# Kernel tuning notes

Measured on AMD Instinct MI355X. Metric: run time of the kernel, lower is better.

## Reference

```python
import jax, jax.numpy as jnp
import numpy as np


def setup_inputs() -> dict:
    key = jax.random.key(0)
    k1, k2, k3, k4 = jax.random.split(key, 4)
    B, S, D_IN, D_OUT = 4, 4096, 768, 128
    x = jax.random.normal(k1, (B, S, D_IN), dtype=jnp.float32)
    # torch Linear(d_in, d_out) weight is [d_out, d_in]; we store transposed [d_in, d_out]
    scale = 1.0 / np.sqrt(D_IN)
    Wq = jax.random.normal(k2, (D_IN, D_OUT), dtype=jnp.float32) * scale
    Wk = jax.random.normal(k3, (D_IN, D_OUT), dtype=jnp.float32) * scale
    Wv = jax.random.normal(k4, (D_IN, D_OUT), dtype=jnp.float32) * scale
    return {"x": x, "Wq": Wq, "Wk": Wk, "Wv": Wv}


def reference(x, Wq, Wk, Wv):
    # x: [B, S, d_in]; Wq/Wk/Wv: [d_in, d_out]
    B, S, _ = x.shape
    q = jnp.einsum('bsd,de->bse', x, Wq)
    k = jnp.einsum('bsd,de->bse', x, Wk)
    v = jnp.einsum('bsd,de->bse', x, Wv)
    d_out = k.shape[-1]
    scores = jnp.einsum('bqe,bke->bqk', q, k)  # [B, S, S]
    causal = jnp.tril(jnp.ones((S, S), dtype=bool))  # True where attention allowed
    scores = jnp.where(causal[None], scores, -jnp.inf)
    attn = jax.nn.softmax(scores / jnp.sqrt(jnp.float32(d_out)), axis=-1)
    # dropout prob is 0.0 -> identity
    return jnp.einsum('bqk,bke->bqe', attn, v)
```

## Files before the change

### kernel.cpp

```cpp
#include <hip/hip_runtime.h>
#include <stdint.h>

typedef unsigned short u16;
typedef uint32_t u32;
typedef __bf16 bf16;
typedef bf16 bf16x8 __attribute__((ext_vector_type(8)));
typedef bf16 bf16x4 __attribute__((ext_vector_type(4)));
typedef short s16x4 __attribute__((ext_vector_type(4)));
typedef float f32x4 __attribute__((ext_vector_type(4)));
typedef uint32_t u32x4 __attribute__((ext_vector_type(4)));

#define S_LEN 4096
#define D_IN 768
#define D_OUT 128
#define NB 4
#define M_TOTAL (NB * S_LEN)

static __device__ __forceinline__ u16 f2bf(float f) {
    union { float f; uint32_t u; } c; c.f = f;
    return (u16)((c.u + 0x7FFFu + ((c.u >> 16) & 1u)) >> 16);
}
static __device__ __forceinline__ float bf2f_lo(uint32_t w) { return __uint_as_float(w << 16); }
static __device__ __forceinline__ float bf2f_hi(uint32_t w) { return __uint_as_float(w & 0xFFFF0000u); }

static __device__ __forceinline__ bf16x8 ld8(const u16* p) {
    union { u32x4 v; bf16x8 b; } c;
    c.v = *reinterpret_cast<const u32x4*>(p);
    return c.b;
}

static __device__ __forceinline__ f32x4 mfma16(bf16x8 a, bf16x8 b, f32x4 c) {
    return __builtin_amdgcn_mfma_f32_16x16x32_bf16(a, b, c, 0, 0, 0);
}

static __device__ __forceinline__ f32x4 mfma16k16(uint2 a, uint2 b, f32x4 c) {
#if defined(__HIP_DEVICE_COMPILE__)
#if __has_builtin(__builtin_amdgcn_mfma_f32_16x16x16_bf16)
    union { uint2 u; bf16x4 v; } ca, cb; ca.u = a; cb.u = b;
    return __builtin_amdgcn_mfma_f32_16x16x16_bf16(ca.v, cb.v, c, 0, 0, 0);
#else
    union { uint2 u; s16x4 v; } ca, cb; ca.u = a; cb.u = b;
    return __builtin_amdgcn_mfma_f32_16x16x16bf16_1k(ca.v, cb.v, c, 0, 0, 0);
#endif
#else
    (void)a; (void)b;
    return c;
#endif
}

static __device__ __forceinline__ void gload16(const void* g, void* l) {
    __builtin_amdgcn_global_load_lds((const __attribute__((address_space(1))) uint32_t*)g,
                                     (__attribute__((address_space(3))) uint32_t*)l, 16, 0, 0);
}

static __device__ __forceinline__ float bpermf(int addr, float v) {
    return __int_as_float(__builtin_amdgcn_ds_bpermute(addr, __float_as_int(v)));
}
static __device__ __forceinline__ u32 pk2(float a, float b) {
    return __builtin_amdgcn_perm(__float_as_uint(b), __float_as_uint(a), 0x07060302u);
}

__global__ __launch_bounds__(256) void wt_kernel(const float* __restrict__ Wq, const float* __restrict__ Wk,
                                                 const float* __restrict__ Wv, u16* __restrict__ Wt) {
    __shared__ u16 tl[128][40];
    const int w = blockIdx.x / 24;
    const int kc = (blockIdx.x % 24) * 32;
    const float* W = (w == 0) ? Wq : (w == 1) ? Wk : Wv;
#pragma unroll
    for (int p = 0; p < 4; ++p) {
        int kr = p * 8 + (threadIdx.x >> 5);
        int nc = (threadIdx.x & 31) * 4;
        float4 v = *reinterpret_cast<const float4*>(W + (size_t)(kc + kr) * D_OUT + nc);
        tl[nc + 0][kr] = f2bf(v.x); tl[nc + 1][kr] = f2bf(v.y);
        tl[nc + 2][kr] = f2bf(v.z); tl[nc + 3][kr] = f2bf(v.w);
    }
    __syncthreads();
    const int n = threadIdx.x >> 1, kh = (threadIdx.x & 1) * 16;
    u32x4* dst = reinterpret_cast<u32x4*>(Wt + (size_t)w * D_OUT * D_IN + (size_t)n * D_IN + kc + kh);
    const u32x4* src = reinterpret_cast<const u32x4*>(&tl[n][kh]);
    dst[0] = src[0];
    dst[1] = src[1];
}

__global__ __launch_bounds__(256) void qkv_kernel(const float* __restrict__ x, const u16* __restrict__ Wt,
                                                  u16* __restrict__ Qb, u16* __restrict__ Kb,
                                                  u16* __restrict__ Vt) {
    __shared__ __align__(16) u16 wslab[2][192 * 32];
    __shared__ __align__(16) float xslab[2][64 * 32];
    const int wave = threadIdx.x >> 6, lane = threadIdx.x & 63;
    const int r = lane & 15, g = lane >> 4;
    const int m0 = blockIdx.x * 64;
    const int h = blockIdx.y;

    f32x4 acc[3][4];
#pragma unroll
    for (int y = 0; y < 3; ++y)
#pragma unroll
        for (int f = 0; f < 4; ++f) acc[y][f] = f32x4{0.f, 0.f, 0.f, 0.f};

    auto stageW = [&](int bb, int kk) {
#pragma unroll
        for (int i = 0; i < 3; ++i) {
            int c = i * 4 + wave;
            int rr = c * 16 + (lane >> 2);
            int gr = (rr >> 6) * 128 + h * 64 + (rr & 63);
            const u16* src = Wt + (size_t)gr * D_IN + kk * 32 + (((lane & 3) ^ (rr & 3)) * 8);
            gload16(src, &wslab[bb][c * 512]);
        }
    };
    auto stageX = [&](int bb, int kk) {
#pragma unroll
        for (int i = 0; i < 2; ++i) {
            int c = i * 4 + wave;
            int row = c * 8 + (lane >> 3);
            const float* src = x + (size_t)(m0 + row) * D_IN + kk * 32 + (((lane & 7) ^ (row & 7)) * 4);
            gload16(src, &xslab[bb][c * 256]);
        }
    };

    stageW(0, 0);
    stageX(0, 0);
    int buf = 0;
    const int arow = wave * 16 + r;
    for (int kk = 0; kk < 24; ++kk) {
        int kn = (kk + 1 < 24) ? kk + 1 : 0;
        stageX(buf ^ 1, kn);
        stageW(buf ^ 1, kn);
        asm volatile("s_waitcnt vmcnt(5)" ::: "memory");
        __builtin_amdgcn_sched_barrier(0);
        __builtin_amdgcn_s_barrier();
        f32x4 xa0 = *reinterpret_cast<const f32x4*>(&xslab[buf][arow * 32 + (((2 * g) ^ (arow & 7)) * 4)]);
        f32x4 xa1 = *reinterpret_cast<const f32x4*>(&xslab[buf][arow * 32 + (((2 * g + 1) ^ (arow & 7)) * 4)]);
        union { u16 u[8]; bf16x8 bv; } af;
#pragma unroll
        for (int t = 0; t < 4; ++t) { af.u[t] = f2bf(xa0[t]); af.u[4 + t] = f2bf(xa1[t]); }
#pragma unroll
        for (int y = 0; y < 3; ++y)
#pragma unroll
            for (int f = 0; f < 4; ++f) {
                int rr = y * 64 + f * 16 + r;
                bf16x8 wf = ld8(&wslab[buf][rr * 32 + ((g ^ (r & 3)) * 8)]);
                acc[y][f] = mfma16(af.bv, wf, acc[y][f]);
            }
        __builtin_amdgcn_s_barrier();
        buf ^= 1;
    }
    asm volatile("s_waitcnt vmcnt(0)" ::: "memory");

    const float QSC = 0.1275174366f;
#pragma unroll
    for (int f = 0; f < 4; ++f)
#pragma unroll
        for (int i = 0; i < 4; ++i) {
            int mrow = m0 + wave * 16 + 4 * g + i;
            int col = h * 64 + f * 16 + r;
            Qb[(size_t)mrow * D_OUT + col] = f2bf(acc[0][f][i] * QSC);
            Kb[(size_t)mrow * D_OUT + col] = f2bf(acc[1][f][i]);
            Vt[((size_t)((mrow >> 12) * D_OUT + col)) * S_LEN + (mrow & 4095)] = f2bf(acc[2][f][i]);
        }
}

__global__ __launch_bounds__(512, 2) void attn_kernel(const u16* __restrict__ Qb, const u16* __restrict__ Kb,
                                                      const u16* __restrict__ Vt, u16* __restrict__ Po,
                                                      float* __restrict__ Pml, float* __restrict__ out,
                                                      int nsplit) {
    __shared__ __align__(16) u16 kbuf[2][64 * 128];
    __shared__ __align__(16) u16 vbuf[2][128 * 64];

    const int wave = threadIdx.x >> 6, lane = threadIdx.x & 63;
    const int r = lane & 15, g = lane >> 4;
    const int n = (int)blockIdx.x;
    const int b = (n & 7) >> 1;
    const int rem = ((n >> 3) << 1) | (n & 1);
    const int s = rem >> 4;
    const int xh = rem & 15;
    const int t = (2 * s < nsplit) ? (15 - xh) : xh;
    const int nj = 4 * t + 4;
    if (s >= nj) return;
    const int qw0 = t * 256 + wave * 32;

    const u16* Kp = Kb + (size_t)b * S_LEN * D_OUT;
    const u16* Vp = Vt + (size_t)b * D_OUT * S_LEN;

    bf16x8 qf[2][4];
#pragma unroll
    for (int rb = 0; rb < 2; ++rb)
#pragma unroll
        for (int kk = 0; kk < 4; ++kk)
            qf[rb][kk] = ld8(Qb + ((size_t)(b * S_LEN + qw0 + rb * 16 + r)) * D_OUT + kk * 32 + 8 * g);

    f32x4 o[2][8];
    float l_[2];
#pragma unroll
    for (int rb = 0; rb < 2; ++rb) {
#pragma unroll
        for (int f = 0; f < 8; ++f) o[rb][f] = f32x4{0.f, 0.f, 0.f, 0.f};
        l_[rb] = 0.f;
    }

    const int lx16 = (lane ^ 16) * 4, lx32 = (lane ^ 32) * 4;

    auto stageK = [&](int bb, int k0) {
#pragma unroll
        for (int i = 0; i < 2; ++i) {
            int c = i * 8 + wave;
            int row = c * 4 + (lane >> 4);
            const u16* src = Kp + (size_t)(k0 + row) * D_OUT + (((lane & 15) ^ (row & 7)) * 8);
            gload16(src, &kbuf[bb][c * 512]);
        }
    };
    auto stageV = [&](int bb, int k0) {
#pragma unroll
        for (int i = 0; i < 2; ++i) {
            int c = i * 8 + wave;
            int row = c * 8 + (lane >> 3);
            const u16* src = Vp + (size_t)row * S_LEN + k0 + (((lane & 7) ^ (row & 7)) * 8);
            gload16(src, &vbuf[bb][c * 512]);
        }
    };

    stageK(0, s * 64);
    stageV(0, s * 64);
    int buf = 0;
    for (int j = s; j < nj; j += nsplit) {
        const int k0 = j * 64;
        asm volatile("s_waitcnt vmcnt(0)" ::: "memory");
        __builtin_amdgcn_sched_barrier(0);
        __builtin_amdgcn_s_barrier();
        const int j2 = j + nsplit;
        if (j2 < nj) {
            stageK(buf ^ 1, j2 * 64);
            stageV(buf ^ 1, j2 * 64);
        }

        f32x4 sv[2][4];
#pragma unroll
        for (int rb = 0; rb < 2; ++rb)
#pragma unroll
            for (int f = 0; f < 4; ++f) sv[rb][f] = f32x4{0.f, 0.f, 0.f, 0.f};
        __builtin_amdgcn_s_setprio(1);
#pragma unroll
        for (int kk = 0; kk < 4; ++kk)
#pragma unroll
            for (int f = 0; f < 4; ++f) {
                bf16x8 kf = ld8(&kbuf[buf][(f * 16 + r) * 128 + (((kk * 4 + g) ^ (r & 7)) * 8)]);
                sv[0][f] = mfma16(kf, qf[0][kk], sv[0][f]);
                sv[1][f] = mfma16(kf, qf[1][kk], sv[1][f]);
            }
        __builtin_amdgcn_s_setprio(0);

        uint2 pb[2][4];
#pragma unroll
        for (int rb = 0; rb < 2; ++rb) {
            const int qrb = qw0 + rb * 16;
            const int q = qrb + r;
            if (k0 + 63 > qrb) {
#pragma unroll
                for (int f = 0; f < 4; ++f)
#pragma unroll
                    for (int i = 0; i < 4; ++i)
                        if (k0 + 16 * f + 4 * g + i > q) sv[rb][f][i] = -1e30f;
            }
            float r0 = 0.f;
#pragma unroll
            for (int f = 0; f < 4; ++f)
#pragma unroll
                for (int i = 0; i < 4; ++i) {
                    float p = __builtin_amdgcn_exp2f(sv[rb][f][i]);
                    sv[rb][f][i] = p;
                    r0 += p;
                }
            l_[rb] += r0;
#pragma unroll
            for (int kb = 0; kb < 4; ++kb) {
                pb[rb][kb].x = pk2(sv[rb][kb][0], sv[rb][kb][1]);
                pb[rb][kb].y = pk2(sv[rb][kb][2], sv[rb][kb][3]);
            }
        }

        __builtin_amdgcn_s_setprio(1);
#pragma unroll
        for (int kb = 0; kb < 4; ++kb) {
            const int vs = ((2 * kb + (g >> 1)) ^ (r & 7)) * 8 + 4 * (g & 1);
#pragma unroll
            for (int f = 0; f < 8; ++f) {
                uint2 vf = *reinterpret_cast<const uint2*>(&vbuf[buf][(f * 16 + r) * 64 + vs]);
                o[0][f] = mfma16k16(vf, pb[0][kb], o[0][f]);
                o[1][f] = mfma16k16(vf, pb[1][kb], o[1][f]);
            }
        }
        __builtin_amdgcn_s_setprio(0);
        buf ^= 1;
    }
    asm volatile("s_waitcnt vmcnt(0)" ::: "memory");

    l_[0] += bpermf(lx16, l_[0]);
    l_[1] += bpermf(lx16, l_[1]);
    l_[0] += bpermf(lx32, l_[0]);
    l_[1] += bpermf(lx32, l_[1]);

    if (nsplit == 1) {
#pragma unroll
        for (int rb = 0; rb < 2; ++rb) {
            float inv = 1.0f / l_[rb];
            float* orow = out + ((size_t)(b * S_LEN + qw0 + rb * 16 + r)) * D_OUT;
#pragma unroll
            for (int f = 0; f < 8; ++f) {
                float4 v;
                v.x = o[rb][f][0] * inv; v.y = o[rb][f][1] * inv;
                v.z = o[rb][f][2] * inv; v.w = o[rb][f][3] * inv;
                *reinterpret_cast<float4*>(orow + 16 * f + 4 * g) = v;
            }
        }
    } else {
        const int pt = (b * 16 + t) * nsplit + s;
        u16* po = Po + (size_t)pt * (256 * 128);
        float* pml = Pml + (size_t)pt * 512;
#pragma unroll
        for (int rb = 0; rb < 2; ++rb) {
            u16* chunk0 = po + (size_t)((wave * 2 + rb) * 8) * 256 + lane * 4;
#pragma unroll
            for (int f = 0; f < 8; ++f) {
                u32 w0 = (u32)f2bf(o[rb][f][0]) | ((u32)f2bf(o[rb][f][1]) << 16);
                u32 w1 = (u32)f2bf(o[rb][f][2]) | ((u32)f2bf(o[rb][f][3]) << 16);
                uint2 ww; ww.x = w0; ww.y = w1;
                *reinterpret_cast<uint2*>(chunk0 + f * 256) = ww;
            }
            if (g == 0) {
                const int row = wave * 32 + rb * 16 + r;
                pml[row * 2 + 0] = 0.f;
                pml[row * 2 + 1] = l_[rb];
            }
        }
    }
}

__global__ __launch_bounds__(256) void merge_kernel(const u16* __restrict__ Po, const float* __restrict__ Pml,
                                                    float* __restrict__ out, int nsplit) {
    const int gr = blockIdx.x * 16 + (threadIdx.x >> 4);
    const int c0 = (threadIdx.x & 15) * 8;
    const int b = gr >> 12, rr = gr & 4095;
    const int t = rr >> 8, row = rr & 255;
    const int ns = min(nsplit, 4 * t + 4);
    const size_t pbase = (size_t)(b * 16 + t) * nsplit;

    const int wv = row >> 5, rbm = (row >> 4) & 1, r_ = row & 15;
    const int fm = c0 >> 4, g0 = (c0 >> 2) & 3;
    const size_t coff = (size_t)((wv * 2 + rbm) * 8 + fm) * 256;

    float L = 0.f;
#pragma unroll
    for (int s = 0; s < 8; ++s)
        if (s < ns) L += Pml[(pbase + s) * 512 + row * 2 + 1];
    const float inv = 1.0f / L;

    float acc[8];
#pragma unroll
    for (int k = 0; k < 8; ++k) acc[k] = 0.f;
#pragma unroll
    for (int s = 0; s < 8; ++s) {
        if (s < ns) {
            const u16* chunk = Po + (pbase + s) * (256 * 128) + coff;
            uint2 pv0 = *reinterpret_cast<const uint2*>(chunk + (g0 * 16 + r_) * 4);
            uint2 pv1 = *reinterpret_cast<const uint2*>(chunk + ((g0 + 1) * 16 + r_) * 4);
            acc[0] += bf2f_lo(pv0.x); acc[1] += bf2f_hi(pv0.x);
            acc[2] += bf2f_lo(pv0.y); acc[3] += bf2f_hi(pv0.y);
            acc[4] += bf2f_lo(pv1.x); acc[5] += bf2f_hi(pv1.x);
            acc[6] += bf2f_lo(pv1.y); acc[7] += bf2f_hi(pv1.y);
        }
    }
    float* op = out + (size_t)gr * D_OUT + c0;
    float4 v0, v1;
    v0.x = acc[0] * inv; v0.y = acc[1] * inv; v0.z = acc[2] * inv; v0.w = acc[3] * inv;
    v1.x = acc[4] * inv; v1.y = acc[5] * inv; v1.z = acc[6] * inv; v1.w = acc[7] * inv;
    *reinterpret_cast<float4*>(op) = v0;
    *reinterpret_cast<float4*>(op + 4) = v1;
}

extern "C" void kernel_launch(void* const* d_in, const int* in_sizes, int n_in,
                              void* d_out, int out_size, void* d_ws, size_t ws_size,
                              hipStream_t stream) {
    const float* x  = (const float*)d_in[0];
    const float* Wq = (const float*)d_in[1];
    const float* Wk = (const float*)d_in[2];
    const float* Wv = (const float*)d_in[3];
    float* out = (float*)d_out;

    u16* Qb = (u16*)d_ws;
    u16* Kb = Qb + (size_t)M_TOTAL * D_OUT;
    u16* Vt = Kb + (size_t)M_TOTAL * D_OUT;
    u16* Wt = Vt + (size_t)M_TOTAL * D_OUT;

    const unsigned long long base = (3ULL * M_TOTAL * D_OUT + 3ULL * D_OUT * D_IN) * 2ULL;
    const unsigned long long per = 4325376ULL;
    int nsplit = 8;
    if (ws_size < base + 8ULL * per) nsplit = 4;
    if (ws_size < base + 4ULL * per) nsplit = 2;
    if (ws_size < base + 2ULL * per) nsplit = 1;

    u16* Po = Wt + (size_t)3 * D_OUT * D_IN;
    float* Pml = (float*)(Po + (size_t)nsplit * 2097152ULL);

    wt_kernel<<<72, 256, 0, stream>>>(Wq, Wk, Wv, Wt);
    qkv_kernel<<<dim3(256, 2), 256, 0, stream>>>(x, Wt, Qb, Kb, Vt);
    attn_kernel<<<16 * nsplit * NB, 512, 0, stream>>>(Qb, Kb, Vt, Po, Pml, out, nsplit);
    if (nsplit > 1)
        merge_kernel<<<M_TOTAL / 16, 256, 0, stream>>>(Po, Pml, out, nsplit);
}
```

Measured before the change: 96.19 us.

## Balance causal attention splits per query tile and halve QKV block rows

Attention work is now split per query tile with a variable number of KV splits that grows with tile index, set by lookup tables, for 115 blocks per batch. Before, every tile used a fixed nsplit and blocks that had no work exited early. This is meant to even out per-block work under the causal mask and fill the GPU better. Separately, the QKV projection kernel now uses 32-row blocks, with wave pairs splitting the output columns, which doubles the grid to improve occupancy. In exchange the merge kernel reads up to 13 partials for the deepest tiles, and the split path needs more workspace; with less workspace it falls back to an unsplit mode.

```diff
diff --git a/kernel.cpp b/kernel.cpp
--- a/kernel.cpp
+++ b/kernel.cpp
@@ -15,6 +15,16 @@
 #define D_OUT 128
 #define NB 4
 #define M_TOTAL (NB * S_LEN)
+#define NPROP 115
+
+__device__ const unsigned char SPLITS_T[16] = {1,2,3,4,4,5,6,7,8,8,9,10,11,12,12,13};
+__device__ const unsigned char OFF_T[16]    = {0,1,3,6,10,14,19,25,32,40,48,57,67,78,90,102};
+__device__ const unsigned char TILE_OF[NPROP] = {
+    0, 1,1, 2,2,2, 3,3,3,3, 4,4,4,4, 5,5,5,5,5, 6,6,6,6,6,6, 7,7,7,7,7,7,7,
+    8,8,8,8,8,8,8,8, 9,9,9,9,9,9,9,9, 10,10,10,10,10,10,10,10,10,
+    11,11,11,11,11,11,11,11,11,11, 12,12,12,12,12,12,12,12,12,12,12,
+    13,13,13,13,13,13,13,13,13,13,13,13, 14,14,14,14,14,14,14,14,14,14,14,14,
+    15,15,15,15,15,15,15,15,15,15,15,15,15};
 
 static __device__ __forceinline__ u16 f2bf(float f) {
     union { float f; uint32_t u; } c; c.f = f;
@@ -86,22 +96,22 @@
                                                   u16* __restrict__ Qb, u16* __restrict__ Kb,
                                                   u16* __restrict__ Vt) {
     __shared__ __align__(16) u16 wslab[2][192 * 32];
-    __shared__ __align__(16) float xslab[2][64 * 32];
+    __shared__ __align__(16) float xslab[2][32 * 32];
     const int wave = threadIdx.x >> 6, lane = threadIdx.x & 63;
     const int r = lane & 15, g = lane >> 4;
-    const int m0 = blockIdx.x * 64;
+    const int m0 = blockIdx.x * 32;
     const int h = blockIdx.y;
 
-    f32x4 acc[3][4];
+    f32x4 acc[3][2];
 #pragma unroll
     for (int y = 0; y < 3; ++y)
 #pragma unroll
-        for (int f = 0; f < 4; ++f) acc[y][f] = f32x4{0.f, 0.f, 0.f, 0.f};
+        for (int f = 0; f < 2; ++f) acc[y][f] = f32x4{0.f, 0.f, 0.f, 0.f};
 
     auto stageW = [&](int bb, int kk) {
 #pragma unroll
         for (int i = 0; i < 3; ++i) {
-            int c = i * 4 + wave;
+            int c = wave * 3 + i;
             int rr = c * 16 + (lane >> 2);
             int gr = (rr >> 6) * 128 + h * 64 + (rr & 63);
             const u16* src = Wt + (size_t)gr * D_IN + kk * 32 + (((lane & 3) ^ (rr & 3)) * 8);
@@ -109,24 +119,22 @@
         }
     };
     auto stageX = [&](int bb, int kk) {
-#pragma unroll
-        for (int i = 0; i < 2; ++i) {
-            int c = i * 4 + wave;
-            int row = c * 8 + (lane >> 3);
-            const float* src = x + (size_t)(m0 + row) * D_IN + kk * 32 + (((lane & 7) ^ (row & 7)) * 4);
-            gload16(src, &xslab[bb][c * 256]);
-        }
+        int c = wave;
+        int row = c * 8 + (lane >> 3);
+        const float* src = x + (size_t)(m0 + row) * D_IN + kk * 32 + (((lane & 7) ^ (row & 7)) * 4);
+        gload16(src, &xslab[bb][c * 256]);
     };
 
     stageW(0, 0);
     stageX(0, 0);
     int buf = 0;
-    const int arow = wave * 16 + r;
+    const int arow = (wave >> 1) * 16 + r;
+    const int ch = (wave & 1) * 32;
     for (int kk = 0; kk < 24; ++kk) {
         int kn = (kk + 1 < 24) ? kk + 1 : 0;
         stageX(buf ^ 1, kn);
         stageW(buf ^ 1, kn);
-        asm volatile("s_waitcnt vmcnt(5)" ::: "memory");
+        asm volatile("s_waitcnt vmcnt(4)" ::: "memory");
         __builtin_amdgcn_sched_barrier(0);
         __builtin_amdgcn_s_barrier();
         f32x4 xa0 = *reinterpret_cast<const f32x4*>(&xslab[buf][arow * 32 + (((2 * g) ^ (arow & 7)) * 4)]);
@@ -137,8 +145,8 @@
 #pragma unroll
         for (int y = 0; y < 3; ++y)
 #pragma unroll
-            for (int f = 0; f < 4; ++f) {
-                int rr = y * 64 + f * 16 + r;
+            for (int f = 0; f < 2; ++f) {
+                int rr = y * 64 + ch + f * 16 + r;
                 bf16x8 wf = ld8(&wslab[buf][rr * 32 + ((g ^ (r & 3)) * 8)]);
                 acc[y][f] = mfma16(af.bv, wf, acc[y][f]);
             }
@@ -149,11 +157,11 @@
 
     const float QSC = 0.1275174366f;
 #pragma unroll
-    for (int f = 0; f < 4; ++f)
+    for (int f = 0; f < 2; ++f)
 #pragma unroll
         for (int i = 0; i < 4; ++i) {
-            int mrow = m0 + wave * 16 + 4 * g + i;
-            int col = h * 64 + f * 16 + r;
+            int mrow = m0 + (wave >> 1) * 16 + 4 * g + i;
+            int col = h * 64 + ch + f * 16 + r;
             Qb[(size_t)mrow * D_OUT + col] = f2bf(acc[0][f][i] * QSC);
             Kb[(size_t)mrow * D_OUT + col] = f2bf(acc[1][f][i]);
             Vt[((size_t)((mrow >> 12) * D_OUT + col)) * S_LEN + (mrow & 4095)] = f2bf(acc[2][f][i]);
@@ -163,20 +171,24 @@
 __global__ __launch_bounds__(512, 2) void attn_kernel(const u16* __restrict__ Qb, const u16* __restrict__ Kb,
                                                       const u16* __restrict__ Vt, u16* __restrict__ Po,
                                                       float* __restrict__ Pml, float* __restrict__ out,
-                                                      int nsplit) {
+                                                      int mode) {
     __shared__ __align__(16) u16 kbuf[2][64 * 128];
     __shared__ __align__(16) u16 vbuf[2][128 * 64];
 
     const int wave = threadIdx.x >> 6, lane = threadIdx.x & 63;
     const int r = lane & 15, g = lane >> 4;
     const int n = (int)blockIdx.x;
-    const int b = (n & 7) >> 1;
-    const int rem = ((n >> 3) << 1) | (n & 1);
-    const int s = rem >> 4;
-    const int xh = rem & 15;
-    const int t = (2 * s < nsplit) ? (15 - xh) : xh;
+    int b, t, s, sp;
+    if (mode) {
+        b = n / NPROP;
+        const int idx = n - b * NPROP;
+        t = TILE_OF[idx];
+        s = idx - OFF_T[t];
+        sp = SPLITS_T[t];
+    } else {
+        b = n >> 4; t = n & 15; s = 0; sp = 1;
+    }
     const int nj = 4 * t + 4;
-    if (s >= nj) return;
     const int qw0 = t * 256 + wave * 32;
 
     const u16* Kp = Kb + (size_t)b * S_LEN * D_OUT;
@@ -222,12 +234,12 @@
     stageK(0, s * 64);
     stageV(0, s * 64);
     int buf = 0;
-    for (int j = s; j < nj; j += nsplit) {
+    for (int j = s; j < nj; j += sp) {
         const int k0 = j * 64;
         asm volatile("s_waitcnt vmcnt(0)" ::: "memory");
         __builtin_amdgcn_sched_barrier(0);
         __builtin_amdgcn_s_barrier();
-        const int j2 = j + nsplit;
+        const int j2 = j + sp;
         if (j2 < nj) {
             stageK(buf ^ 1, j2 * 64);
             stageV(buf ^ 1, j2 * 64);
@@ -299,7 +311,7 @@
     l_[0] += bpermf(lx32, l_[0]);
     l_[1] += bpermf(lx32, l_[1]);
 
-    if (nsplit == 1) {
+    if (!mode) {
 #pragma unroll
         for (int rb = 0; rb < 2; ++rb) {
             float inv = 1.0f / l_[rb];
@@ -313,9 +325,8 @@
             }
         }
     } else {
-        const int pt = (b * 16 + t) * nsplit + s;
-        u16* po = Po + (size_t)pt * (256 * 128);
-        float* pml = Pml + (size_t)pt * 512;
+        u16* po = Po + (size_t)n * (256 * 128);
+        float* pml = Pml + (size_t)n * 512;
 #pragma unroll
         for (int rb = 0; rb < 2; ++rb) {
             u16* chunk0 = po + (size_t)((wave * 2 + rb) * 8) * 256 + lane * 4;
@@ -336,38 +347,33 @@
 }
 
 __global__ __launch_bounds__(256) void merge_kernel(const u16* __restrict__ Po, const float* __restrict__ Pml,
-                                                    float* __restrict__ out, int nsplit) {
+                                                    float* __restrict__ out) {
     const int gr = blockIdx.x * 16 + (threadIdx.x >> 4);
     const int c0 = (threadIdx.x & 15) * 8;
     const int b = gr >> 12, rr = gr & 4095;
     const int t = rr >> 8, row = rr & 255;
-    const int ns = min(nsplit, 4 * t + 4);
-    const size_t pbase = (size_t)(b * 16 + t) * nsplit;
+    const int ns = SPLITS_T[t];
+    const size_t pbase = (size_t)b * NPROP + OFF_T[t];
 
     const int wv = row >> 5, rbm = (row >> 4) & 1, r_ = row & 15;
     const int fm = c0 >> 4, g0 = (c0 >> 2) & 3;
     const size_t coff = (size_t)((wv * 2 + rbm) * 8 + fm) * 256;
 
     float L = 0.f;
-#pragma unroll
-    for (int s = 0; s < 8; ++s)
-        if (s < ns) L += Pml[(pbase + s) * 512 + row * 2 + 1];
+    for (int s = 0; s < ns; ++s) L += Pml[(pbase + s) * 512 + row * 2 + 1];
     const float inv = 1.0f / L;
 
     float acc[8];
 #pragma unroll
     for (int k = 0; k < 8; ++k) acc[k] = 0.f;
-#pragma unroll
-    for (int s = 0; s < 8; ++s) {
-        if (s < ns) {
-            const u16* chunk = Po + (pbase + s) * (256 * 128) + coff;
-            uint2 pv0 = *reinterpret_cast<const uint2*>(chunk + (g0 * 16 + r_) * 4);
-            uint2 pv1 = *reinterpret_cast<const uint2*>(chunk + ((g0 + 1) * 16 + r_) * 4);
-            acc[0] += bf2f_lo(pv0.x); acc[1] += bf2f_hi(pv0.x);
-            acc[2] += bf2f_lo(pv0.y); acc[3] += bf2f_hi(pv0.y);
-            acc[4] += bf2f_lo(pv1.x); acc[5] += bf2f_hi(pv1.x);
-            acc[6] += bf2f_lo(pv1.y); acc[7] += bf2f_hi(pv1.y);
-        }
+    for (int s = 0; s < ns; ++s) {
+        const u16* chunk = Po + (pbase + s) * (256 * 128) + coff;
+        uint2 pv0 = *reinterpret_cast<const uint2*>(chunk + (g0 * 16 + r_) * 4);
+        uint2 pv1 = *reinterpret_cast<const uint2*>(chunk + ((g0 + 1) * 16 + r_) * 4);
+        acc[0] += bf2f_lo(pv0.x); acc[1] += bf2f_hi(pv0.x);
+        acc[2] += bf2f_lo(pv0.y); acc[3] += bf2f_hi(pv0.y);
+        acc[4] += bf2f_lo(pv1.x); acc[5] += bf2f_hi(pv1.x);
+        acc[6] += bf2f_lo(pv1.y); acc[7] += bf2f_hi(pv1.y);
     }
     float* op = out + (size_t)gr * D_OUT + c0;
     float4 v0, v1;
@@ -392,18 +398,16 @@
     u16* Wt = Vt + (size_t)M_TOTAL * D_OUT;
 
     const unsigned long long base = (3ULL * M_TOTAL * D_OUT + 3ULL * D_OUT * D_IN) * 2ULL;
-    const unsigned long long per = 4325376ULL;
-    int nsplit = 8;
-    if (ws_size < base + 8ULL * per) nsplit = 4;
-    if (ws_size < base + 4ULL * per) nsplit = 2;
-    if (ws_size < base + 2ULL * per) nsplit = 1;
+    const unsigned long long perP = 256ULL * 128 * 2 + 512ULL * 4;
+    const int nblk = NPROP * NB;
+    const int mode = (ws_size >= base + (unsigned long long)nblk * perP) ? 1 : 0;
 
     u16* Po = Wt + (size_t)3 * D_OUT * D_IN;
-    float* Pml = (float*)(Po + (size_t)nsplit * 2097152ULL);
+    float* Pml = (float*)(Po + (size_t)nblk * (256 * 128));
 
     wt_kernel<<<72, 256, 0, stream>>>(Wq, Wk, Wv, Wt);
-    qkv_kernel<<<dim3(256, 2), 256, 0, stream>>>(x, Wt, Qb, Kb, Vt);
-    attn_kernel<<<16 * nsplit * NB, 512, 0, stream>>>(Qb, Kb, Vt, Po, Pml, out, nsplit);
-    if (nsplit > 1)
-        merge_kernel<<<M_TOTAL / 16, 256, 0, stream>>>(Po, Pml, out, nsplit);
-}
+    qkv_kernel<<<dim3(512, 2), 256, 0, stream>>>(x, Wt, Qb, Kb, Vt);
+    attn_kernel<<<mode ? nblk : 16 * NB, 512, 0, stream>>>(Qb, Kb, Vt, Po, Pml, out, mode);
+    if (mode)
+        merge_kernel<<<M_TOTAL / 16, 256, 0, stream>>>(Po, Pml, out);
+}
```

Result: no change. 94.84 us (-1.4%).
